# Optimization experiments

Measured on AMD Instinct MI355X. Metric: run time of the kernel, lower is better.

Reference implementation:

```python
import jax, jax.numpy as jnp
import numpy as np

EPS = 1e-5


def _proj(x, W, b, g, beta):
    # Linear + LayerNorm over last axis (ProjectionFCNN with norm=True)
    h = jnp.einsum('bld,dh->blh', x, W) + b
    mu = jnp.mean(h, axis=-1, keepdims=True)
    var = jnp.var(h, axis=-1, keepdims=True)
    return (h - mu) * jax.lax.rsqrt(var + EPS) * g + beta


def setup_inputs() -> dict:
    key = jax.random.key(0)
    ks = jax.random.split(key, 8)
    B, L, DQ, DKV, H = 8, 2048, 512, 768, 512
    s = 0.02
    return {
        'query_sequence': jax.random.normal(ks[0], (B, L, DQ), jnp.float32),
        'key_value_sequence': jax.random.normal(ks[1], (B, L, DKV), jnp.float32),
        'Wq': jax.random.normal(ks[2], (DQ, H), jnp.float32) * s,
        'bq': jnp.zeros((H,), jnp.float32),
        'gq': jnp.ones((H,), jnp.float32),
        'betaq': jnp.zeros((H,), jnp.float32),
        'Wk': jax.random.normal(ks[3], (DKV, H), jnp.float32) * s,
        'bk': jnp.zeros((H,), jnp.float32),
        'gk': jnp.ones((H,), jnp.float32),
        'betak': jnp.zeros((H,), jnp.float32),
        'Wv': jax.random.normal(ks[4], (DKV, DQ), jnp.float32) * s,
        'bv': jnp.zeros((DQ,), jnp.float32),
        'gv': jnp.ones((DQ,), jnp.float32),
        'betav': jnp.zeros((DQ,), jnp.float32),
    }


def reference(query_sequence, key_value_sequence, Wq, bq, gq, betaq,
              Wk, bk, gk, betak, Wv, bv, gv, betav):
    query = _proj(query_sequence, Wq, bq, gq, betaq)          # [b, L, H]
    k = _proj(key_value_sequence, Wk, bk, gk, betak)          # [b, l, H]
    v = _proj(key_value_sequence, Wv, bv, gv, betav)          # [b, l, DQ]
    # attn_score: 'b l c, b L c -> b l L'; softmax over last (query) axis
    attn = jax.nn.softmax(jnp.einsum('blc,bLc->blL', k, query), axis=-1)
    out = jnp.einsum('blL,bLc->blc', attn, v)                 # [b, l, DQ]
    return out + query_sequence
```

## Files before the change

### kernel.cpp

```cpp
#include <hip/hip_runtime.h>

typedef _Float16 f16;
typedef _Float16 f16x4 __attribute__((ext_vector_type(4)));
typedef _Float16 f16x8 __attribute__((ext_vector_type(8)));
typedef float f32x4 __attribute__((ext_vector_type(4)));
typedef unsigned int u32;

#define NB   8
#define SEQ  2048
#define DQ_  512
#define DKV_ 768
#define HD_  512

__device__ __forceinline__ void gll16(const void* g, void* l) {
  __builtin_amdgcn_global_load_lds(
      (const __attribute__((address_space(1))) u32*)g,
      (__attribute__((address_space(3))) u32*)l, 16, 0, 0);
}

__global__ __launch_bounds__(256) void cast_transpose(const float* __restrict__ in,
                                                      f16* __restrict__ out,
                                                      int K, int N) {
  int i = blockIdx.x * 256 + threadIdx.x;
  if (i >= K * N) return;
  int n = i / K, k = i % K;
  out[i] = (f16)in[k * N + n];
}

__global__ __launch_bounds__(512) void proj_ln(
    const float* __restrict__ xq, const float* __restrict__ xkv,
    const f16* __restrict__ wqt, const f16* __restrict__ wkt, const f16* __restrict__ wvt,
    const float* __restrict__ bq, const float* __restrict__ gq, const float* __restrict__ beq,
    const float* __restrict__ bk, const float* __restrict__ gk, const float* __restrict__ bek,
    const float* __restrict__ bv, const float* __restrict__ gv, const float* __restrict__ bev,
    f16* __restrict__ outq, f16* __restrict__ outk, f16* __restrict__ outvt)
{
  __shared__ char smem[36864 + 4096 + 512];
  f16* Xs    = (f16*)smem;
  f16* trans = (f16*)smem;
  float* red = (float*)(smem + 36864);
  float* mus = (float*)(smem + 36864 + 4096);
  float* rss = mus + 64;

  const int proj = blockIdx.x >> 8;
  const int tile = blockIdx.x & 255;
  const float* X; const f16* Wt; const float *bias, *gam, *bet; f16* out; int KD;
  if (proj == 0)      { X = xq;  Wt = wqt; bias = bq; gam = gq; bet = beq; out = outq;  KD = 512; }
  else if (proj == 1) { X = xkv; Wt = wkt; bias = bk; gam = gk; bet = bek; out = outk;  KD = 768; }
  else                { X = xkv; Wt = wvt; bias = bv; gam = gv; bet = bev; out = outvt; KD = 768; }

  const int row0 = tile * 64;
  const int tid = threadIdx.x;
  const int w = tid >> 6;
  const int lane = tid & 63;
  const int g = lane >> 4, tt = lane & 15;

  const int rX = tid >> 3, cX = (tid & 7) * 16;
  const float* xrow = X + (size_t)(row0 + rX) * KD + cX;
  const f16* wrow[4];
  #pragma unroll
  for (int n = 0; n < 4; ++n)
    wrow[n] = Wt + (size_t)(w * 64 + n * 16 + tt) * KD + g * 8;

  f32x4 acc[4][4] = {};

  const int nstrip = KD >> 7;
  float4 xa = *(const float4*)(xrow);
  float4 xb = *(const float4*)(xrow + 4);
  float4 xc = *(const float4*)(xrow + 8);
  float4 xd = *(const float4*)(xrow + 12);
  const float* xp = xrow + 128;

  for (int st = 0; st < nstrip; ++st) {
    {
      f16x8 h0, h1;
      h0[0] = (f16)xa.x; h0[1] = (f16)xa.y; h0[2] = (f16)xa.z; h0[3] = (f16)xa.w;
      h0[4] = (f16)xb.x; h0[5] = (f16)xb.y; h0[6] = (f16)xb.z; h0[7] = (f16)xb.w;
      h1[0] = (f16)xc.x; h1[1] = (f16)xc.y; h1[2] = (f16)xc.z; h1[3] = (f16)xc.w;
      h1[4] = (f16)xd.x; h1[5] = (f16)xd.y; h1[6] = (f16)xd.z; h1[7] = (f16)xd.w;
      *(f16x8*)&Xs[rX * 148 + cX]     = h0;
      *(f16x8*)&Xs[rX * 148 + cX + 8] = h1;
    }
    __syncthreads();
    if (st + 1 < nstrip) {
      xa = *(const float4*)(xp);
      xb = *(const float4*)(xp + 4);
      xc = *(const float4*)(xp + 8);
      xd = *(const float4*)(xp + 12);
      xp += 128;
    }
    #pragma unroll
    for (int s = 0; s < 4; ++s) {
      f16x8 af[4], bf[4];
      #pragma unroll
      for (int n = 0; n < 4; ++n)
        bf[n] = *(const f16x8*)(wrow[n] + s * 32);
      #pragma unroll
      for (int m = 0; m < 4; ++m)
        af[m] = *(const f16x8*)&Xs[(m * 16 + tt) * 148 + s * 32 + g * 8];
      #pragma unroll
      for (int n = 0; n < 4; ++n)
        #pragma unroll
        for (int m = 0; m < 4; ++m)
          acc[m][n] = __builtin_amdgcn_mfma_f32_16x16x32_f16(af[m], bf[n], acc[m][n], 0, 0, 0);
    }
    #pragma unroll
    for (int n = 0; n < 4; ++n) wrow[n] += 128;
    __syncthreads();
  }

  float bias4[4], gam4[4], bet4[4];
  #pragma unroll
  for (int n = 0; n < 4; ++n) {
    int c = w * 64 + n * 16 + tt;
    bias4[n] = bias[c]; gam4[n] = gam[c]; bet4[n] = bet[c];
  }
  float rsum[4][4], rsq[4][4];
  #pragma unroll
  for (int m = 0; m < 4; ++m)
    #pragma unroll
    for (int j = 0; j < 4; ++j) { rsum[m][j] = 0.f; rsq[m][j] = 0.f; }
  #pragma unroll
  for (int m = 0; m < 4; ++m)
    #pragma unroll
    for (int n = 0; n < 4; ++n)
      #pragma unroll
      for (int j = 0; j < 4; ++j) {
        float h = acc[m][n][j] + bias4[n];
        acc[m][n][j] = h;
        rsum[m][j] += h; rsq[m][j] += h * h;
      }
  #pragma unroll
  for (int mk = 1; mk < 16; mk <<= 1)
    #pragma unroll
    for (int m = 0; m < 4; ++m)
      #pragma unroll
      for (int j = 0; j < 4; ++j) {
        rsum[m][j] += __shfl_xor(rsum[m][j], mk);
        rsq[m][j]  += __shfl_xor(rsq[m][j], mk);
      }
  if (tt == 0) {
    #pragma unroll
    for (int m = 0; m < 4; ++m)
      #pragma unroll
      for (int j = 0; j < 4; ++j) {
        int r = m * 16 + g * 4 + j;
        red[(r * 8 + w) * 2 + 0] = rsum[m][j];
        red[(r * 8 + w) * 2 + 1] = rsq[m][j];
      }
  }
  __syncthreads();
  if (tid < 64) {
    float s = 0.f, sq = 0.f;
    #pragma unroll
    for (int w2 = 0; w2 < 8; ++w2) {
      s  += red[(tid * 8 + w2) * 2 + 0];
      sq += red[(tid * 8 + w2) * 2 + 1];
    }
    float mu = s * (1.f / 512.f);
    float var = sq * (1.f / 512.f) - mu * mu;
    mus[tid] = mu;
    rss[tid] = rsqrtf(var + 1e-5f);
  }
  __syncthreads();
  #pragma unroll
  for (int m = 0; m < 4; ++m)
    #pragma unroll
    for (int j = 0; j < 4; ++j) {
      int r = m * 16 + g * 4 + j;
      float mu = mus[r], rs = rss[r];
      #pragma unroll
      for (int n = 0; n < 4; ++n)
        acc[m][n][j] = (acc[m][n][j] - mu) * rs * gam4[n] + bet4[n];
    }

  if (proj != 2) {
    #pragma unroll
    for (int m = 0; m < 4; ++m)
      #pragma unroll
      for (int j = 0; j < 4; ++j) {
        int r = row0 + m * 16 + g * 4 + j;
        #pragma unroll
        for (int n = 0; n < 4; ++n)
          out[(size_t)r * 512 + w * 64 + n * 16 + tt] = (f16)acc[m][n][j];
      }
  } else {
    const int bch = row0 >> 11, l0 = row0 & 2047;
    __syncthreads();
    for (int half = 0; half < 2; ++half) {
      if ((w >> 2) == half) {
        #pragma unroll
        for (int m = 0; m < 4; ++m)
          #pragma unroll
          for (int n = 0; n < 4; ++n)
            #pragma unroll
            for (int j = 0; j < 4; ++j)
              trans[((w & 3) * 64 + n * 16 + tt) * 72 + (m * 16 + g * 4 + j)] =
                  (f16)acc[m][n][j];
      }
      __syncthreads();
      {
        int c = tid >> 1, ii = tid & 1;
        size_t gb = (size_t)bch * (512 * 2048) + (size_t)(half * 256 + c) * 2048
                    + l0 + ii * 32;
        #pragma unroll
        for (int q2 = 0; q2 < 4; ++q2)
          *(f16x8*)&out[gb + q2 * 8] = *(const f16x8*)&trans[c * 72 + ii * 32 + q2 * 8];
      }
      __syncthreads();
    }
  }
}

template <bool RESID, typename CT, int K, int tilesM, int tilesN, int N>
__global__ __launch_bounds__(256) void gemm_nt(
    const f16* __restrict__ A, const f16* __restrict__ Bt,
    CT* __restrict__ C, const float* __restrict__ resid)
{
  constexpr size_t sA = (size_t)SEQ * K;
  constexpr size_t sB = (size_t)tilesN * 128 * K;
  constexpr size_t sC = (size_t)SEQ * N;
  constexpr int bpb = tilesM * tilesN;
  constexpr int nwg = bpb * NB;
  __shared__ f16 As[128 * 64];
  __shared__ f16 Bs[128 * 64];
  const int orig = blockIdx.x;
  const int bid = (orig & 7) * (nwg / 8) + (orig >> 3);
  const int b = bid / bpb;
  const int t = bid - b * bpb;
  const int tm = t % tilesM, tn = t / tilesM;
  const int tid = threadIdx.x, w = tid >> 6, lane = tid & 63;
  const int wr = w >> 1, wc = w & 1;
  const int g = lane >> 4, tt = lane & 15;

  const f16* Ab  = A  + (size_t)b * sA + (size_t)tm * 128 * K;
  const f16* Btb = Bt + (size_t)b * sB + (size_t)tn * 128 * K;
  const f16* aS[4]; const f16* bS[4]; int ld[4];
  #pragma unroll
  for (int i = 0; i < 4; ++i) {
    int oi = i * 4096 + tid * 16;
    int r = oi >> 7, c = (oi >> 4) & 7, cs = c ^ (r & 7);
    ld[i] = oi;
    aS[i] = Ab  + (size_t)r * K + cs * 8;
    bS[i] = Btb + (size_t)r * K + cs * 8;
  }
  int aOff[4][2], bOff[4][2];
  #pragma unroll
  for (int m = 0; m < 4; ++m) {
    int R = wr * 64 + m * 16 + tt;
    #pragma unroll
    for (int kk = 0; kk < 2; ++kk)
      aOff[m][kk] = R * 64 + (((kk * 4 + g) ^ (R & 7)) * 8);
  }
  #pragma unroll
  for (int n = 0; n < 4; ++n) {
    int R = wc * 64 + n * 16 + tt;
    #pragma unroll
    for (int kk = 0; kk < 2; ++kk)
      bOff[n][kk] = R * 64 + (((kk * 4 + g) ^ (R & 7)) * 8);
  }

  f32x4 acc[4][4] = {};
  #pragma unroll
  for (int kt = 0; kt < K; kt += 64) {
    #pragma unroll
    for (int i = 0; i < 4; ++i) {
      gll16(aS[i] + kt, (char*)As + ld[i]);
      gll16(bS[i] + kt, (char*)Bs + ld[i]);
    }
    __syncthreads();
    #pragma unroll
    for (int kk = 0; kk < 2; ++kk) {
      f16x8 af[4], bf[4];
      #pragma unroll
      for (int m = 0; m < 4; ++m) af[m] = *(const f16x8*)&As[aOff[m][kk]];
      #pragma unroll
      for (int n = 0; n < 4; ++n) bf[n] = *(const f16x8*)&Bs[bOff[n][kk]];
      #pragma unroll
      for (int n = 0; n < 4; ++n)
        #pragma unroll
        for (int m = 0; m < 4; ++m)
          acc[m][n] = __builtin_amdgcn_mfma_f32_16x16x32_f16(af[m], bf[n], acc[m][n], 0, 0, 0);
    }
    __syncthreads();
  }
  const size_t Cb = (size_t)b * sC;
  #pragma unroll
  for (int m = 0; m < 4; ++m)
    #pragma unroll
    for (int j = 0; j < 4; ++j) {
      int r = tm * 128 + wr * 64 + m * 16 + g * 4 + j;
      #pragma unroll
      for (int n = 0; n < 4; ++n) {
        int c = tn * 128 + wc * 64 + n * 16 + tt;
        size_t idx = Cb + (size_t)r * N + c;
        float v = acc[m][n][j];
        if (RESID) v += resid[idx];
        C[idx] = (CT)v;
      }
    }
}

__global__ __launch_bounds__(256) void softmax_rows(f16* __restrict__ SP)
{
  __shared__ float sred[4];
  const size_t row = blockIdx.x;
  f16x8* Pr = (f16x8*)(SP + row * 2048);
  const int tid = threadIdx.x, w = tid >> 6, lane = tid & 63;
  f16x8 v = Pr[tid];
  float f[8];
  #pragma unroll
  for (int j = 0; j < 8; ++j) f[j] = (float)v[j];
  float mx = f[0];
  #pragma unroll
  for (int j = 1; j < 8; ++j) mx = fmaxf(mx, f[j]);
  #pragma unroll
  for (int mk = 1; mk < 64; mk <<= 1) mx = fmaxf(mx, __shfl_xor(mx, mk));
  if (lane == 0) sred[w] = mx;
  __syncthreads();
  mx = fmaxf(fmaxf(sred[0], sred[1]), fmaxf(sred[2], sred[3]));
  __syncthreads();
  float e[8], s = 0.f;
  #pragma unroll
  for (int j = 0; j < 8; ++j) { e[j] = __expf(f[j] - mx); s += e[j]; }
  #pragma unroll
  for (int mk = 1; mk < 64; mk <<= 1) s += __shfl_xor(s, mk);
  if (lane == 0) sred[w] = s;
  __syncthreads();
  s = sred[0] + sred[1] + sred[2] + sred[3];
  float inv = 1.f / s;
  f16x8 p;
  #pragma unroll
  for (int j = 0; j < 8; ++j) p[j] = (f16)(e[j] * inv);
  Pr[tid] = p;
}

extern "C" void kernel_launch(void* const* d_in, const int* in_sizes, int n_in,
                              void* d_out, int out_size, void* d_ws, size_t ws_size,
                              hipStream_t stream) {
  const float* qs   = (const float*)d_in[0];
  const float* kv   = (const float*)d_in[1];
  const float* Wq   = (const float*)d_in[2];
  const float* bq   = (const float*)d_in[3];
  const float* gq   = (const float*)d_in[4];
  const float* beq  = (const float*)d_in[5];
  const float* Wk   = (const float*)d_in[6];
  const float* bk   = (const float*)d_in[7];
  const float* gk   = (const float*)d_in[8];
  const float* bek  = (const float*)d_in[9];
  const float* Wv   = (const float*)d_in[10];
  const float* bv   = (const float*)d_in[11];
  const float* gv   = (const float*)d_in[12];
  const float* bev  = (const float*)d_in[13];
  float* out = (float*)d_out;

  char* ws = (char*)d_ws;
  f16* q16  = (f16*)(ws + 0);
  f16* k16  = (f16*)(ws + 16777216);
  f16* vt   = (f16*)(ws + 33554432);
  f16* Wqt  = (f16*)(ws + 50331648);
  f16* Wkt  = (f16*)(ws + 50855936);
  f16* Wvt  = (f16*)(ws + 51642368);
  f16* S    = (f16*)(ws + 52428800);

  cast_transpose<<<1024, 256, 0, stream>>>(Wq, Wqt, 512, 512);
  cast_transpose<<<1536, 256, 0, stream>>>(Wk, Wkt, 768, 512);
  cast_transpose<<<1536, 256, 0, stream>>>(Wv, Wvt, 768, 512);

  proj_ln<<<768, 512, 0, stream>>>(qs, kv, Wqt, Wkt, Wvt,
                                   bq, gq, beq, bk, gk, bek, bv, gv, bev,
                                   q16, k16, vt);

  gemm_nt<false, f16, 512, 16, 16, 2048><<<2048, 256, 0, stream>>>(
      k16, q16, S, nullptr);

  softmax_rows<<<16384, 256, 0, stream>>>(S);

  gemm_nt<true, float, 2048, 16, 4, 512><<<512, 256, 0, stream>>>(
      S, vt, out, qs);
}
```

Before: 360.7 us.

## Double-buffer X tile in proj_ln and split rows across 16 waves

The projection+LayerNorm kernel now runs 1024 threads per block, with 16 waves arranged 2x8 so each wave computes 32 rows by 64 columns instead of 64 by 64. The X strip is double-buffered in LDS, so the conversion and store of the next strip happen after the current MFMAs, and one barrier per strip is removed. The aim is more latency hiding and fewer syncs per strip. In exchange each wave reloads the same W fragments from global memory, doubling W traffic per block, and the larger block may limit how many blocks fit per CU.

```diff
diff --git a/kernel.cpp b/kernel.cpp
--- a/kernel.cpp
+++ b/kernel.cpp
@@ -27,7 +27,7 @@
   out[i] = (f16)in[k * N + n];
 }
 
-__global__ __launch_bounds__(512) void proj_ln(
+__global__ __launch_bounds__(1024) void proj_ln(
     const float* __restrict__ xq, const float* __restrict__ xkv,
     const f16* __restrict__ wqt, const f16* __restrict__ wkt, const f16* __restrict__ wvt,
     const float* __restrict__ bq, const float* __restrict__ gq, const float* __restrict__ beq,
@@ -36,7 +36,8 @@
     f16* __restrict__ outq, f16* __restrict__ outk, f16* __restrict__ outvt)
 {
   __shared__ char smem[36864 + 4096 + 512];
-  f16* Xs    = (f16*)smem;
+  f16* Xs0   = (f16*)smem;
+  f16* Xs1   = (f16*)(smem + 17408);
   f16* trans = (f16*)smem;
   float* red = (float*)(smem + 36864);
   float* mus = (float*)(smem + 36864 + 4096);
@@ -52,76 +53,80 @@
   const int row0 = tile * 64;
   const int tid = threadIdx.x;
   const int w = tid >> 6;
+  const int wr = w >> 3, wc = w & 7;
   const int lane = tid & 63;
   const int g = lane >> 4, tt = lane & 15;
 
-  const int rX = tid >> 3, cX = (tid & 7) * 16;
-  const float* xrow = X + (size_t)(row0 + rX) * KD + cX;
+  const int rX = tid >> 4, cX = (tid & 15) * 8;
+  const float* xp = X + (size_t)(row0 + rX) * KD + cX;
   const f16* wrow[4];
   #pragma unroll
   for (int n = 0; n < 4; ++n)
-    wrow[n] = Wt + (size_t)(w * 64 + n * 16 + tt) * KD + g * 8;
-
-  f32x4 acc[4][4] = {};
+    wrow[n] = Wt + (size_t)(wc * 64 + n * 16 + tt) * KD + g * 8;
+
+  f32x4 acc[2][4] = {};
 
   const int nstrip = KD >> 7;
-  float4 xa = *(const float4*)(xrow);
-  float4 xb = *(const float4*)(xrow + 4);
-  float4 xc = *(const float4*)(xrow + 8);
-  float4 xd = *(const float4*)(xrow + 12);
-  const float* xp = xrow + 128;
+  {
+    float4 a = *(const float4*)(xp);
+    float4 b = *(const float4*)(xp + 4);
+    xp += 128;
+    f16x8 h;
+    h[0] = (f16)a.x; h[1] = (f16)a.y; h[2] = (f16)a.z; h[3] = (f16)a.w;
+    h[4] = (f16)b.x; h[5] = (f16)b.y; h[6] = (f16)b.z; h[7] = (f16)b.w;
+    *(f16x8*)&Xs0[rX * 136 + cX] = h;
+  }
+  __syncthreads();
 
   for (int st = 0; st < nstrip; ++st) {
-    {
-      f16x8 h0, h1;
-      h0[0] = (f16)xa.x; h0[1] = (f16)xa.y; h0[2] = (f16)xa.z; h0[3] = (f16)xa.w;
-      h0[4] = (f16)xb.x; h0[5] = (f16)xb.y; h0[6] = (f16)xb.z; h0[7] = (f16)xb.w;
-      h1[0] = (f16)xc.x; h1[1] = (f16)xc.y; h1[2] = (f16)xc.z; h1[3] = (f16)xc.w;
-      h1[4] = (f16)xd.x; h1[5] = (f16)xd.y; h1[6] = (f16)xd.z; h1[7] = (f16)xd.w;
-      *(f16x8*)&Xs[rX * 148 + cX]     = h0;
-      *(f16x8*)&Xs[rX * 148 + cX + 8] = h1;
-    }
-    __syncthreads();
-    if (st + 1 < nstrip) {
+    f16* cur = (st & 1) ? Xs1 : Xs0;
+    f16* nxt = (st & 1) ? Xs0 : Xs1;
+    float4 xa, xb;
+    const bool more = (st + 1 < nstrip);
+    if (more) {
       xa = *(const float4*)(xp);
       xb = *(const float4*)(xp + 4);
-      xc = *(const float4*)(xp + 8);
-      xd = *(const float4*)(xp + 12);
       xp += 128;
     }
     #pragma unroll
     for (int s = 0; s < 4; ++s) {
-      f16x8 af[4], bf[4];
+      f16x8 af[2], bf[4];
       #pragma unroll
       for (int n = 0; n < 4; ++n)
         bf[n] = *(const f16x8*)(wrow[n] + s * 32);
       #pragma unroll
-      for (int m = 0; m < 4; ++m)
-        af[m] = *(const f16x8*)&Xs[(m * 16 + tt) * 148 + s * 32 + g * 8];
+      for (int m = 0; m < 2; ++m)
+        af[m] = *(const f16x8*)&cur[(wr * 32 + m * 16 + tt) * 136 + s * 32 + g * 8];
       #pragma unroll
       for (int n = 0; n < 4; ++n)
         #pragma unroll
-        for (int m = 0; m < 4; ++m)
+        for (int m = 0; m < 2; ++m)
           acc[m][n] = __builtin_amdgcn_mfma_f32_16x16x32_f16(af[m], bf[n], acc[m][n], 0, 0, 0);
     }
     #pragma unroll
     for (int n = 0; n < 4; ++n) wrow[n] += 128;
+    if (more) {
+      f16x8 h;
+      h[0] = (f16)xa.x; h[1] = (f16)xa.y; h[2] = (f16)xa.z; h[3] = (f16)xa.w;
+      h[4] = (f16)xb.x; h[5] = (f16)xb.y; h[6] = (f16)xb.z; h[7] = (f16)xb.w;
+      *(f16x8*)&nxt[rX * 136 + cX] = h;
+    }
     __syncthreads();
   }
 
   float bias4[4], gam4[4], bet4[4];
   #pragma unroll
   for (int n = 0; n < 4; ++n) {
-    int c = w * 64 + n * 16 + tt;
+    int c = wc * 64 + n * 16 + tt;
     bias4[n] = bias[c]; gam4[n] = gam[c]; bet4[n] = bet[c];
   }
-  float rsum[4][4], rsq[4][4];
-  #pragma unroll
-  for (int m = 0; m < 4; ++m)
+  float rsum[2][4], rsq[2][4];
+  #pragma unroll
+  for (int m = 0; m < 2; ++m)
     #pragma unroll
     for (int j = 0; j < 4; ++j) { rsum[m][j] = 0.f; rsq[m][j] = 0.f; }
   #pragma unroll
-  for (int m = 0; m < 4; ++m)
+  for (int m = 0; m < 2; ++m)
     #pragma unroll
     for (int n = 0; n < 4; ++n)
       #pragma unroll
@@ -133,7 +138,7 @@
   #pragma unroll
   for (int mk = 1; mk < 16; mk <<= 1)
     #pragma unroll
-    for (int m = 0; m < 4; ++m)
+    for (int m = 0; m < 2; ++m)
       #pragma unroll
       for (int j = 0; j < 4; ++j) {
         rsum[m][j] += __shfl_xor(rsum[m][j], mk);
@@ -141,12 +146,12 @@
       }
   if (tt == 0) {
     #pragma unroll
-    for (int m = 0; m < 4; ++m)
+    for (int m = 0; m < 2; ++m)
       #pragma unroll
       for (int j = 0; j < 4; ++j) {
-        int r = m * 16 + g * 4 + j;
-        red[(r * 8 + w) * 2 + 0] = rsum[m][j];
-        red[(r * 8 + w) * 2 + 1] = rsq[m][j];
+        int r = wr * 32 + m * 16 + g * 4 + j;
+        red[(r * 8 + wc) * 2 + 0] = rsum[m][j];
+        red[(r * 8 + wc) * 2 + 1] = rsq[m][j];
       }
   }
   __syncthreads();
@@ -164,10 +169,10 @@
   }
   __syncthreads();
   #pragma unroll
-  for (int m = 0; m < 4; ++m)
+  for (int m = 0; m < 2; ++m)
     #pragma unroll
     for (int j = 0; j < 4; ++j) {
-      int r = m * 16 + g * 4 + j;
+      int r = wr * 32 + m * 16 + g * 4 + j;
       float mu = mus[r], rs = rss[r];
       #pragma unroll
       for (int n = 0; n < 4; ++n)
@@ -176,36 +181,36 @@
 
   if (proj != 2) {
     #pragma unroll
-    for (int m = 0; m < 4; ++m)
+    for (int m = 0; m < 2; ++m)
       #pragma unroll
       for (int j = 0; j < 4; ++j) {
-        int r = row0 + m * 16 + g * 4 + j;
+        int r = row0 + wr * 32 + m * 16 + g * 4 + j;
         #pragma unroll
         for (int n = 0; n < 4; ++n)
-          out[(size_t)r * 512 + w * 64 + n * 16 + tt] = (f16)acc[m][n][j];
+          out[(size_t)r * 512 + wc * 64 + n * 16 + tt] = (f16)acc[m][n][j];
       }
   } else {
     const int bch = row0 >> 11, l0 = row0 & 2047;
     __syncthreads();
     for (int half = 0; half < 2; ++half) {
-      if ((w >> 2) == half) {
-        #pragma unroll
-        for (int m = 0; m < 4; ++m)
+      if ((wc >> 2) == half) {
+        #pragma unroll
+        for (int m = 0; m < 2; ++m)
           #pragma unroll
           for (int n = 0; n < 4; ++n)
             #pragma unroll
             for (int j = 0; j < 4; ++j)
-              trans[((w & 3) * 64 + n * 16 + tt) * 72 + (m * 16 + g * 4 + j)] =
+              trans[((wc & 3) * 64 + n * 16 + tt) * 72 + (wr * 32 + m * 16 + g * 4 + j)] =
                   (f16)acc[m][n][j];
       }
       __syncthreads();
       {
-        int c = tid >> 1, ii = tid & 1;
+        int c = tid >> 2, ii = tid & 3;
         size_t gb = (size_t)bch * (512 * 2048) + (size_t)(half * 256 + c) * 2048
-                    + l0 + ii * 32;
-        #pragma unroll
-        for (int q2 = 0; q2 < 4; ++q2)
-          *(f16x8*)&out[gb + q2 * 8] = *(const f16x8*)&trans[c * 72 + ii * 32 + q2 * 8];
+                    + l0 + ii * 16;
+        #pragma unroll
+        for (int q2 = 0; q2 < 2; ++q2)
+          *(f16x8*)&out[gb + q2 * 8] = *(const f16x8*)&trans[c * 72 + ii * 16 + q2 * 8];
       }
       __syncthreads();
     }
@@ -367,9 +372,9 @@
   cast_transpose<<<1536, 256, 0, stream>>>(Wk, Wkt, 768, 512);
   cast_transpose<<<1536, 256, 0, stream>>>(Wv, Wvt, 768, 512);
 
-  proj_ln<<<768, 512, 0, stream>>>(qs, kv, Wqt, Wkt, Wvt,
-                                   bq, gq, beq, bk, gk, bek, bv, gv, bev,
-                                   q16, k16, vt);
+  proj_ln<<<768, 1024, 0, stream>>>(qs, kv, Wqt, Wkt, Wvt,
+                                    bq, gq, beq, bk, gk, bek, bv, gv, bev,
+                                    q16, k16, vt);
 
   gemm_nt<false, f16, 512, 16, 16, 2048><<<2048, 256, 0, stream>>>(
       k16, q16, S, nullptr);
```

Result: slower. 392.7 us (+8.9%).
